# Kernel optimization log

Hardware: AMD Instinct MI355X
Metric: run time of the kernel (lower is better)

## Reference

```python
import jax, jax.numpy as jnp
import numpy as np


def setup_inputs() -> dict:
    key = jax.random.key(0)
    k1, k2 = jax.random.split(key)
    STATE_LEN, SEQ_LEN, D = 8192, 8192, 1024
    user_emb = jax.random.normal(k1, (STATE_LEN, D), dtype=jnp.float32)
    id_emb = jax.random.normal(k2, (SEQ_LEN, D), dtype=jnp.float32)
    return {"user_emb": user_emb, "id_emb": id_emb}


def reference(user_emb, id_emb):
    # attn_energies[i, j] = user_emb[i] . id_emb[j]  -> single GEMM
    energies = jnp.einsum('id,jd->ij', user_emb, id_emb)  # [state_len, seq_len]
    # F.softmax on 2D tensor defaults to dim=1 (rows)
    return jax.nn.softmax(energies, axis=-1)
```

## Files before the change

kernel.cpp:

```cpp
#include <hip/hip_runtime.h>
#include <hip/hip_bf16.h>
#include <stdint.h>

typedef __attribute__((ext_vector_type(8))) short bf16x8;
typedef __attribute__((ext_vector_type(4))) float f32x4;

typedef const __attribute__((address_space(1))) void* gas_ptr;
typedef __attribute__((address_space(3))) void* lds_ptr_t;

__device__ __forceinline__ unsigned short f32_to_bf16_rtn(float x) {
    unsigned u = __float_as_uint(x);
    u += 0x7FFFu + ((u >> 16) & 1u);
    return (unsigned short)(u >> 16);
}
__device__ __forceinline__ float bf16_bits_to_f32(unsigned short h) {
    return __uint_as_float(((unsigned)h) << 16);
}

__global__ __launch_bounds__(256) void split_hi_lo(
    const float* __restrict__ A, const float* __restrict__ B,
    unsigned short* __restrict__ Ahi, unsigned short* __restrict__ Alo,
    unsigned short* __restrict__ Bhi, unsigned short* __restrict__ Blo, int n4)
{
    int i = blockIdx.x * 256 + threadIdx.x;
    if (i >= n4) return;
    float4 a = ((const float4*)A)[i];
    float4 b = ((const float4*)B)[i];
    ushort4 h, l;

    h.x = f32_to_bf16_rtn(a.x); l.x = f32_to_bf16_rtn(a.x - bf16_bits_to_f32(h.x));
    h.y = f32_to_bf16_rtn(a.y); l.y = f32_to_bf16_rtn(a.y - bf16_bits_to_f32(h.y));
    h.z = f32_to_bf16_rtn(a.z); l.z = f32_to_bf16_rtn(a.z - bf16_bits_to_f32(h.z));
    h.w = f32_to_bf16_rtn(a.w); l.w = f32_to_bf16_rtn(a.w - bf16_bits_to_f32(h.w));
    ((ushort4*)Ahi)[i] = h; ((ushort4*)Alo)[i] = l;

    h.x = f32_to_bf16_rtn(b.x); l.x = f32_to_bf16_rtn(b.x - bf16_bits_to_f32(h.x));
    h.y = f32_to_bf16_rtn(b.y); l.y = f32_to_bf16_rtn(b.y - bf16_bits_to_f32(h.y));
    h.z = f32_to_bf16_rtn(b.z); l.z = f32_to_bf16_rtn(b.z - bf16_bits_to_f32(h.z));
    h.w = f32_to_bf16_rtn(b.w); l.w = f32_to_bf16_rtn(b.w - bf16_bits_to_f32(h.w));
    ((ushort4*)Bhi)[i] = h; ((ushort4*)Blo)[i] = l;
}

__global__ __launch_bounds__(256) void gemm_presplit(
    const __hip_bfloat16* __restrict__ Ahi, const __hip_bfloat16* __restrict__ Alo,
    const __hip_bfloat16* __restrict__ Bhi, const __hip_bfloat16* __restrict__ Blo,
    float* __restrict__ out, int M, int N, int K)
{
    __shared__ char sm[32768];
    const int tid  = threadIdx.x;
    const int lane = tid & 63;
    const int w    = tid >> 6;
    const int bm = blockIdx.y, bn = blockIdx.x;
    const int wm = (w >> 1) * 64;
    const int wn = (w & 1) * 64;

    f32x4 acc[4][4] = {};

    const int sfetch = (tid & 3) ^ ((tid >> 3) & 3);
    const size_t offA = (size_t)(bm * 128 + (tid >> 2)) * K + sfetch * 8;
    const size_t offB = (size_t)(bn * 128 + (tid >> 2)) * K + sfetch * 8;
    const __hip_bfloat16* pAh = Ahi + offA;
    const __hip_bfloat16* pAl = Alo + offA;
    const __hip_bfloat16* pBh = Bhi + offB;
    const __hip_bfloat16* pBl = Blo + offB;
    const size_t half = (size_t)64 * K;
    char* dst0 = sm + tid * 16;

    const int rA = lane & 15;
    const int ca = (lane >> 4) ^ ((lane >> 1) & 3);
    const char* aP = sm +         (wm + rA) * 64 + ca * 16;
    const char* bP = sm + 16384 + (wn + rA) * 64 + ca * 16;

    for (int k0 = 0; k0 < K; k0 += 32) {
        __syncthreads();
        __builtin_amdgcn_global_load_lds((gas_ptr)(pAh + k0),        (lds_ptr_t)(dst0),         16, 0, 0);
        __builtin_amdgcn_global_load_lds((gas_ptr)(pAh + half + k0), (lds_ptr_t)(dst0 + 4096),  16, 0, 0);
        __builtin_amdgcn_global_load_lds((gas_ptr)(pAl + k0),        (lds_ptr_t)(dst0 + 8192),  16, 0, 0);
        __builtin_amdgcn_global_load_lds((gas_ptr)(pAl + half + k0), (lds_ptr_t)(dst0 + 12288), 16, 0, 0);
        __builtin_amdgcn_global_load_lds((gas_ptr)(pBh + k0),        (lds_ptr_t)(dst0 + 16384), 16, 0, 0);
        __builtin_amdgcn_global_load_lds((gas_ptr)(pBh + half + k0), (lds_ptr_t)(dst0 + 20480), 16, 0, 0);
        __builtin_amdgcn_global_load_lds((gas_ptr)(pBl + k0),        (lds_ptr_t)(dst0 + 24576), 16, 0, 0);
        __builtin_amdgcn_global_load_lds((gas_ptr)(pBl + half + k0), (lds_ptr_t)(dst0 + 28672), 16, 0, 0);
        __syncthreads();

        bf16x8 bh[4], bl[4];
#pragma unroll
        for (int j = 0; j < 4; ++j) {
            bh[j] = *(const bf16x8*)(bP + j * 1024);
            bl[j] = *(const bf16x8*)(bP + j * 1024 + 8192);
        }
#pragma unroll
        for (int i = 0; i < 4; ++i) {
            bf16x8 ah = *(const bf16x8*)(aP + i * 1024);
            bf16x8 al = *(const bf16x8*)(aP + i * 1024 + 8192);
#pragma unroll
            for (int j = 0; j < 4; ++j) {
                acc[i][j] = __builtin_amdgcn_mfma_f32_16x16x32_bf16(ah, bh[j], acc[i][j], 0, 0, 0);
                acc[i][j] = __builtin_amdgcn_mfma_f32_16x16x32_bf16(al, bh[j], acc[i][j], 0, 0, 0);
                acc[i][j] = __builtin_amdgcn_mfma_f32_16x16x32_bf16(ah, bl[j], acc[i][j], 0, 0, 0);
            }
        }
    }

    const int r0 = bm * 128 + wm + ((lane >> 4) << 2);
    const int c0 = bn * 128 + wn + rA;
#pragma unroll
    for (int i = 0; i < 4; ++i)
#pragma unroll
        for (int j = 0; j < 4; ++j)
#pragma unroll
            for (int r = 0; r < 4; ++r)
                out[(size_t)(r0 + i * 16 + r) * N + (c0 + j * 16)] = acc[i][j][r];
}

__global__ __launch_bounds__(256) void gemm_fallback(
    const float* __restrict__ Af, const float* __restrict__ Bf,
    float* __restrict__ out, int M, int N, int K)
{
    __shared__ char sm[32768];
    const int tid  = threadIdx.x;
    const int lane = tid & 63;
    const int w    = tid >> 6;
    const int bm = blockIdx.y, bn = blockIdx.x;
    const int wm = (w >> 1) * 64;
    const int wn = (w & 1) * 64;

    f32x4 acc[4][4] = {};
    const int sfetch = (tid & 3) ^ ((tid >> 3) & 3);
    const int rA = lane & 15;
    const int ca = (lane >> 4) ^ ((lane >> 1) & 3);
    const char* aP = sm +         (wm + rA) * 64 + ca * 16;
    const char* bP = sm + 16384 + (wn + rA) * 64 + ca * 16;

    for (int k0 = 0; k0 < K; k0 += 32) {
        __syncthreads();
#pragma unroll
        for (int c = 0; c < 4; ++c) {
            const bool isA = (c < 2);
            const int row = ((c & 1) << 6) + (tid >> 2);
            const float* src = (isA ? Af + (size_t)(bm * 128 + row) * K
                                    : Bf + (size_t)(bn * 128 + row) * K)
                               + k0 + ((tid & 3) << 3);
            f32x4 v0 = *(const f32x4*)src;
            f32x4 v1 = *(const f32x4*)(src + 4);
            float vv[8] = {v0.x, v0.y, v0.z, v0.w, v1.x, v1.y, v1.z, v1.w};
            bf16x8 h, l;
#pragma unroll
            for (int j = 0; j < 8; ++j) {
                unsigned short hb = f32_to_bf16_rtn(vv[j]);
                unsigned short lb = f32_to_bf16_rtn(vv[j] - bf16_bits_to_f32(hb));
                h[j] = (short)hb; l[j] = (short)lb;
            }
            const int g = row * 64 + sfetch * 16;
            *(bf16x8*)(sm + (isA ? 0 : 16384) + g) = h;
            *(bf16x8*)(sm + (isA ? 8192 : 24576) + g) = l;
        }
        __syncthreads();

        bf16x8 bh[4], bl[4];
#pragma unroll
        for (int j = 0; j < 4; ++j) {
            bh[j] = *(const bf16x8*)(bP + j * 1024);
            bl[j] = *(const bf16x8*)(bP + j * 1024 + 8192);
        }
#pragma unroll
        for (int i = 0; i < 4; ++i) {
            bf16x8 ah = *(const bf16x8*)(aP + i * 1024);
            bf16x8 al = *(const bf16x8*)(aP + i * 1024 + 8192);
#pragma unroll
            for (int j = 0; j < 4; ++j) {
                acc[i][j] = __builtin_amdgcn_mfma_f32_16x16x32_bf16(ah, bh[j], acc[i][j], 0, 0, 0);
                acc[i][j] = __builtin_amdgcn_mfma_f32_16x16x32_bf16(al, bh[j], acc[i][j], 0, 0, 0);
                acc[i][j] = __builtin_amdgcn_mfma_f32_16x16x32_bf16(ah, bl[j], acc[i][j], 0, 0, 0);
            }
        }
    }

    const int r0 = bm * 128 + wm + ((lane >> 4) << 2);
    const int c0 = bn * 128 + wn + rA;
#pragma unroll
    for (int i = 0; i < 4; ++i)
#pragma unroll
        for (int j = 0; j < 4; ++j)
#pragma unroll
            for (int r = 0; r < 4; ++r)
                out[(size_t)(r0 + i * 16 + r) * N + (c0 + j * 16)] = acc[i][j][r];
}

__global__ __launch_bounds__(256) void softmax_rows_8192(float* __restrict__ d)
{
    const int tid = threadIdx.x;
    __shared__ float smax[4], ssum[4];

    for (int rr = 0; rr < 4; ++rr) {
        const size_t row = (size_t)blockIdx.x * 4 + rr;
        f32x4* p = (f32x4*)(d + row * 8192);
        f32x4 v[8];
        float m = -3.402823466e+38f;
#pragma unroll
        for (int i = 0; i < 8; ++i) {
            v[i] = p[tid + (i << 8)];
            m = fmaxf(m, fmaxf(fmaxf(v[i].x, v[i].y), fmaxf(v[i].z, v[i].w)));
        }
#pragma unroll
        for (int o = 32; o >= 1; o >>= 1) m = fmaxf(m, __shfl_xor(m, o));
        if ((tid & 63) == 0) smax[tid >> 6] = m;
        __syncthreads();
        m = fmaxf(fmaxf(smax[0], smax[1]), fmaxf(smax[2], smax[3]));

        float s = 0.f;
#pragma unroll
        for (int i = 0; i < 8; ++i) {
            v[i].x = __expf(v[i].x - m);
            v[i].y = __expf(v[i].y - m);
            v[i].z = __expf(v[i].z - m);
            v[i].w = __expf(v[i].w - m);
            s += (v[i].x + v[i].y) + (v[i].z + v[i].w);
        }
#pragma unroll
        for (int o = 32; o >= 1; o >>= 1) s += __shfl_xor(s, o);
        if ((tid & 63) == 0) ssum[tid >> 6] = s;
        __syncthreads();
        s = (ssum[0] + ssum[1]) + (ssum[2] + ssum[3]);
        const float r = 1.0f / s;
#pragma unroll
        for (int i = 0; i < 8; ++i) {
            v[i] *= r;
            __builtin_nontemporal_store(v[i], &p[tid + (i << 8)]);
        }
        __syncthreads();
    }
}

extern "C" void kernel_launch(void* const* d_in, const int* in_sizes, int n_in,
                              void* d_out, int out_size, void* d_ws, size_t ws_size,
                              hipStream_t stream)
{
    const float* A = (const float*)d_in[0];
    const float* B = (const float*)d_in[1];
    float* out = (float*)d_out;
    const int K = 1024;
    const int M = in_sizes[0] / K;
    const int N = in_sizes[1] / K;
    const size_t elemsA = (size_t)M * K;
    const size_t elemsB = (size_t)N * K;
    const size_t need = 2 * (elemsA + elemsB) * sizeof(unsigned short);

    dim3 grid(N / 128, M / 128);
    const bool presplit = (ws_size >= need) && (M == N);

    if (presplit) {
        unsigned short* Ahi = (unsigned short*)d_ws;
        unsigned short* Alo = Ahi + elemsA;
        unsigned short* Bhi = Alo + elemsA;
        unsigned short* Blo = Bhi + elemsB;
        const int n4 = (int)(elemsA / 4);
        split_hi_lo<<<(n4 + 255) / 256, 256, 0, stream>>>(A, B, Ahi, Alo, Bhi, Blo, n4);
        gemm_presplit<<<grid, 256, 0, stream>>>(
            (const __hip_bfloat16*)Ahi, (const __hip_bfloat16*)Alo,
            (const __hip_bfloat16*)Bhi, (const __hip_bfloat16*)Blo,
            out, M, N, K);
    } else {
        gemm_fallback<<<grid, 256, 0, stream>>>(A, B, out, M, N, K);
    }
    softmax_rows_8192<<<M / 4, 256, 0, stream>>>(out);
}
```

Measured before the change: 739.1 us.

## Load GEMM fragments directly to registers with double buffering, dropping LDS

Replaces the LDS-staged GEMM loop with per-wave direct global loads of bf16 hi/lo fragments into registers, double-buffered across k-steps so loads for the next slice overlap MFMA work. This removes the two block barriers per k-step and LDS reads. In exchange, each wave refetches data shared with sibling waves, raising L2 traffic, and register usage grows considerably, which may reduce occupancy.

Result: slower. 1.285 ms (+73.8%).

```diff
diff --git a/kernel.cpp b/kernel.cpp
--- a/kernel.cpp
+++ b/kernel.cpp
@@ -4,9 +4,6 @@
 
 typedef __attribute__((ext_vector_type(8))) short bf16x8;
 typedef __attribute__((ext_vector_type(4))) float f32x4;
-
-typedef const __attribute__((address_space(1))) void* gas_ptr;
-typedef __attribute__((address_space(3))) void* lds_ptr_t;
 
 __device__ __forceinline__ unsigned short f32_to_bf16_rtn(float x) {
     unsigned u = __float_as_uint(x);
@@ -41,12 +38,11 @@
     ((ushort4*)Bhi)[i] = h; ((ushort4*)Blo)[i] = l;
 }
 
-__global__ __launch_bounds__(256) void gemm_presplit(
-    const __hip_bfloat16* __restrict__ Ahi, const __hip_bfloat16* __restrict__ Alo,
-    const __hip_bfloat16* __restrict__ Bhi, const __hip_bfloat16* __restrict__ Blo,
+__global__ __launch_bounds__(256) void gemm_direct(
+    const unsigned short* __restrict__ Ahi, const unsigned short* __restrict__ Alo,
+    const unsigned short* __restrict__ Bhi, const unsigned short* __restrict__ Blo,
     float* __restrict__ out, int M, int N, int K)
 {
-    __shared__ char sm[32768];
     const int tid  = threadIdx.x;
     const int lane = tid & 63;
     const int w    = tid >> 6;
@@ -56,51 +52,53 @@
 
     f32x4 acc[4][4] = {};
 
-    const int sfetch = (tid & 3) ^ ((tid >> 3) & 3);
-    const size_t offA = (size_t)(bm * 128 + (tid >> 2)) * K + sfetch * 8;
-    const size_t offB = (size_t)(bn * 128 + (tid >> 2)) * K + sfetch * 8;
-    const __hip_bfloat16* pAh = Ahi + offA;
-    const __hip_bfloat16* pAl = Alo + offA;
-    const __hip_bfloat16* pBh = Bhi + offB;
-    const __hip_bfloat16* pBl = Blo + offB;
-    const size_t half = (size_t)64 * K;
-    char* dst0 = sm + tid * 16;
-
     const int rA = lane & 15;
-    const int ca = (lane >> 4) ^ ((lane >> 1) & 3);
-    const char* aP = sm +         (wm + rA) * 64 + ca * 16;
-    const char* bP = sm + 16384 + (wn + rA) * 64 + ca * 16;
-
-    for (int k0 = 0; k0 < K; k0 += 32) {
-        __syncthreads();
-        __builtin_amdgcn_global_load_lds((gas_ptr)(pAh + k0),        (lds_ptr_t)(dst0),         16, 0, 0);
-        __builtin_amdgcn_global_load_lds((gas_ptr)(pAh + half + k0), (lds_ptr_t)(dst0 + 4096),  16, 0, 0);
-        __builtin_amdgcn_global_load_lds((gas_ptr)(pAl + k0),        (lds_ptr_t)(dst0 + 8192),  16, 0, 0);
-        __builtin_amdgcn_global_load_lds((gas_ptr)(pAl + half + k0), (lds_ptr_t)(dst0 + 12288), 16, 0, 0);
-        __builtin_amdgcn_global_load_lds((gas_ptr)(pBh + k0),        (lds_ptr_t)(dst0 + 16384), 16, 0, 0);
-        __builtin_amdgcn_global_load_lds((gas_ptr)(pBh + half + k0), (lds_ptr_t)(dst0 + 20480), 16, 0, 0);
-        __builtin_amdgcn_global_load_lds((gas_ptr)(pBl + k0),        (lds_ptr_t)(dst0 + 24576), 16, 0, 0);
-        __builtin_amdgcn_global_load_lds((gas_ptr)(pBl + half + k0), (lds_ptr_t)(dst0 + 28672), 16, 0, 0);
-        __syncthreads();
-
-        bf16x8 bh[4], bl[4];
-#pragma unroll
-        for (int j = 0; j < 4; ++j) {
-            bh[j] = *(const bf16x8*)(bP + j * 1024);
-            bl[j] = *(const bf16x8*)(bP + j * 1024 + 8192);
-        }
-#pragma unroll
-        for (int i = 0; i < 4; ++i) {
-            bf16x8 ah = *(const bf16x8*)(aP + i * 1024);
-            bf16x8 al = *(const bf16x8*)(aP + i * 1024 + 8192);
-#pragma unroll
-            for (int j = 0; j < 4; ++j) {
-                acc[i][j] = __builtin_amdgcn_mfma_f32_16x16x32_bf16(ah, bh[j], acc[i][j], 0, 0, 0);
-                acc[i][j] = __builtin_amdgcn_mfma_f32_16x16x32_bf16(al, bh[j], acc[i][j], 0, 0, 0);
-                acc[i][j] = __builtin_amdgcn_mfma_f32_16x16x32_bf16(ah, bl[j], acc[i][j], 0, 0, 0);
-            }
-        }
-    }
+    const int kc = (lane >> 4) << 3;
+    int aoff[4], boff[4];
+#pragma unroll
+    for (int i = 0; i < 4; ++i) {
+        aoff[i] = (bm * 128 + wm + i * 16 + rA) * K + kc;
+        boff[i] = (bn * 128 + wn + i * 16 + rA) * K + kc;
+    }
+
+    bf16x8 ah[2][4], al[2][4], bh[2][4], bl[2][4];
+
+#define LOADF(buf, kk)                                                        \
+    {                                                                         \
+        _Pragma("unroll")                                                     \
+        for (int i = 0; i < 4; ++i) {                                         \
+            ah[buf][i] = *(const bf16x8*)(Ahi + aoff[i] + (kk));              \
+            al[buf][i] = *(const bf16x8*)(Alo + aoff[i] + (kk));              \
+            bh[buf][i] = *(const bf16x8*)(Bhi + boff[i] + (kk));              \
+            bl[buf][i] = *(const bf16x8*)(Blo + boff[i] + (kk));              \
+        }                                                                     \
+    }
+
+#define MFMAS(buf)                                                            \
+    {                                                                         \
+        _Pragma("unroll")                                                     \
+        for (int i = 0; i < 4; ++i) {                                         \
+            _Pragma("unroll")                                                 \
+            for (int j = 0; j < 4; ++j) {                                     \
+                acc[i][j] = __builtin_amdgcn_mfma_f32_16x16x32_bf16(          \
+                    ah[buf][i], bh[buf][j], acc[i][j], 0, 0, 0);              \
+                acc[i][j] = __builtin_amdgcn_mfma_f32_16x16x32_bf16(          \
+                    al[buf][i], bh[buf][j], acc[i][j], 0, 0, 0);              \
+                acc[i][j] = __builtin_amdgcn_mfma_f32_16x16x32_bf16(          \
+                    ah[buf][i], bl[buf][j], acc[i][j], 0, 0, 0);              \
+            }                                                                 \
+        }                                                                     \
+    }
+
+    LOADF(0, 0);
+    for (int k0 = 0; k0 < K; k0 += 64) {
+        LOADF(1, k0 + 32);
+        MFMAS(0);
+        if (k0 + 64 < K) LOADF(0, k0 + 64);
+        MFMAS(1);
+    }
+#undef LOADF
+#undef MFMAS
 
     const int r0 = bm * 128 + wm + ((lane >> 4) << 2);
     const int c0 = bn * 128 + wn + rA;
@@ -256,10 +254,7 @@
         unsigned short* Blo = Bhi + elemsB;
         const int n4 = (int)(elemsA / 4);
         split_hi_lo<<<(n4 + 255) / 256, 256, 0, stream>>>(A, B, Ahi, Alo, Bhi, Blo, n4);
-        gemm_presplit<<<grid, 256, 0, stream>>>(
-            (const __hip_bfloat16*)Ahi, (const __hip_bfloat16*)Alo,
-            (const __hip_bfloat16*)Bhi, (const __hip_bfloat16*)Blo,
-            out, M, N, K);
+        gemm_direct<<<grid, 256, 0, stream>>>(Ahi, Alo, Bhi, Blo, out, M, N, K);
     } else {
         gemm_fallback<<<grid, 256, 0, stream>>>(A, B, out, M, N, K);
     }
```
